# Kernel tuning notes

Measured on AMD Instinct MI355X. Metric: run time of the kernel, lower is better.

The kernel has to match this reference:

```python
import jax, jax.numpy as jnp
import numpy as np

ALPHA, BETA, GAMMA, DELTA = 1.0, 1.0, 1.0, 0.001
DV, DD = 0.5, 1.5
N_INST = 8
EDGES_MAX = 512
EPS = 1e-12


def _safe_norm(sq):
    # sqrt of a sum-of-squares with a tiny eps for grad stability at 0
    return jnp.sqrt(jnp.maximum(sq, 0.0) + EPS)


def _per_image(feat, labels, label_edges):
    # feat: [P, C]; labels, label_edges: [P] int32 in [0, N_INST)
    P, C = feat.shape
    N = N_INST
    counts = jax.ops.segment_sum(jnp.ones((P,), feat.dtype), labels, num_segments=N)  # [N]
    means = jax.ops.segment_sum(feat, labels, num_segments=N) / counts[:, None]       # [N, C]

    # --- variance (pull) loss: per-pixel distance to its cluster mean ---
    d = _safe_norm(jnp.sum((feat - means[labels]) ** 2, axis=-1))  # [P]
    hinge = jax.nn.relu(d - DV) ** 2
    var_loss = jnp.sum(jax.ops.segment_sum(hinge, labels, num_segments=N) / counts) / N

    # --- distance (push) loss between cluster means, upper triangle ---
    diff = means[:, None, :] - means[None, :, :]
    dm = _safe_norm(jnp.sum(diff ** 2, axis=-1))  # [N, N]
    triu = jnp.triu(jnp.ones((N, N), dtype=bool), k=1)
    dist_loss = jnp.sum(jnp.where(triu, jax.nn.relu(2.0 * DD - dm) ** 2, 0.0)) / (N * (N - 1))

    # --- edge loss: first EDGES_MAX boundary pixels per instance (deterministic subsample) ---
    pix = jnp.arange(P, dtype=feat.dtype)
    def first_members(i):
        score = jnp.where(label_edges == i, -pix, -jnp.inf)
        _, idx = jax.lax.top_k(score, EDGES_MAX)
        return idx
    sel = jax.vmap(first_members)(jnp.arange(N))  # [N, E]
    eb = feat[sel.reshape(-1)]                    # [N*E, C]
    sq = jnp.sum(eb ** 2, axis=-1)
    d2 = sq[:, None] + sq[None, :] - 2.0 * (eb @ eb.T)  # [N*E, N*E] squared dists
    pd = _safe_norm(d2)
    pv = jax.nn.relu(2.0 * (DD - DV) - pd) ** 2
    pair = pv.reshape(N, EDGES_MAX, N, EDGES_MAX).sum(axis=(1, 3)) / (EDGES_MAX * EDGES_MAX)
    edge_loss = jnp.sum(jnp.where(triu, pair, 0.0)) / (N * (N - 1))

    # --- regularization on cluster means ---
    reg_loss = jnp.mean(_safe_norm(jnp.sum(means ** 2, axis=-1)))
    return var_loss, dist_loss, edge_loss, reg_loss


def setup_inputs() -> dict:
    key = jax.random.key(0)
    k1, k2, k3 = jax.random.split(key, 3)
    B, C, H, W = 4, 32, 512, 512
    features = jax.random.normal(k1, (B, C, H, W), jnp.float32)
    labels = jax.random.randint(k2, (B, H, W), 0, N_INST, jnp.int32)
    labelEdges = jax.random.randint(k3, (B, H, W), 0, N_INST, jnp.int32)
    return {"features": features, "labels": labels, "labelEdges": labelEdges}


def reference(features, labels, labelEdges):
    B, C, H, W = features.shape
    feat = features.transpose(0, 2, 3, 1).reshape(B, H * W, C)
    lab = labels.reshape(B, -1)
    le = labelEdges.reshape(B, -1)
    v, d, e, r = jax.vmap(_per_image)(feat, lab, le)
    varLoss = ALPHA * jnp.sum(v)
    distLoss = BETA * jnp.sum(d)
    edgeLoss = GAMMA * jnp.sum(e)
    regLoss = DELTA * jnp.sum(r)
    totalLoss = varLoss + distLoss + edgeLoss + regLoss
    return (totalLoss, varLoss, distLoss, edgeLoss, regLoss)
```

## Files before the change

### kernel.cpp

```cpp
#include <hip/hip_runtime.h>

#define NB 4
#define NC 32
#define NPIX 262144
#define NI 8
#define NE 512
#define FEPS 1e-12f

#define WS_SUMS   0
#define WS_CNT    1024
#define WS_HINGE  1056
#define WS_EDGE   1088
#define WS_ZERO_N 1089
#define WS_SEL    2048
#define WS_EB     20480
#define WS_SQ     544768

typedef __bf16 bf16x8 __attribute__((ext_vector_type(8)));
typedef float  f32x4  __attribute__((ext_vector_type(4)));

static __device__ __forceinline__ unsigned short f2bf(float x) {
    unsigned u = __builtin_bit_cast(unsigned, x);
    u += 0x7FFF + ((u >> 16) & 1);
    return (unsigned short)(u >> 16);
}

__global__ __launch_bounds__(256) void k_zero(float* __restrict__ ws) {
    int i = blockIdx.x * 256 + threadIdx.x;
    if (i < WS_ZERO_N) ws[i] = 0.f;
}

__global__ __launch_bounds__(256, 2) void k_seg_sums(const float* __restrict__ feat,
                                                     const int* __restrict__ lab,
                                                     float* __restrict__ sums,
                                                     float* __restrict__ cnts) {
    int tid = threadIdx.x;
    int lane = tid & 63, w = tid >> 6;
    int b = blockIdx.x >> 8, cb = blockIdx.x & 255;
    const float* fb = feat + ((size_t)b * NC + w * 8) * NPIX + cb * 1024;
    const int*   lb = lab + (size_t)b * NPIX + cb * 1024;

    float r[64];
#pragma unroll
    for (int k = 0; k < 64; k++) r[k] = 0.f;
    float cnt[8] = {0.f, 0.f, 0.f, 0.f, 0.f, 0.f, 0.f, 0.f};

#pragma unroll 1
    for (int g = 0; g < 4; g++) {
        int idx = g * 256 + lane * 4;
        int4 lv = *(const int4*)(lb + idx);
        float4 msk[8];
#pragma unroll
        for (int bin = 0; bin < 8; bin++) {
            msk[bin].x = (lv.x == bin) ? 1.f : 0.f;
            msk[bin].y = (lv.y == bin) ? 1.f : 0.f;
            msk[bin].z = (lv.z == bin) ? 1.f : 0.f;
            msk[bin].w = (lv.w == bin) ? 1.f : 0.f;
        }
        if (w == 0) {
#pragma unroll
            for (int bin = 0; bin < 8; bin++)
                cnt[bin] += msk[bin].x + msk[bin].y + msk[bin].z + msk[bin].w;
        }
#pragma unroll
        for (int c = 0; c < 8; c++) {
            float4 f = *(const float4*)(fb + (size_t)c * NPIX + idx);
#pragma unroll
            for (int bin = 0; bin < 8; bin++)
                r[c * 8 + bin] += msk[bin].x * f.x + msk[bin].y * f.y
                                + msk[bin].z * f.z + msk[bin].w * f.w;
        }
    }

#pragma unroll
    for (int half = 32; half >= 1; half >>= 1) {
#pragma unroll
        for (int k = 0; k < half; k++) {
            float t0 = __shfl_xor(r[k], half);
            float t1 = __shfl_xor(r[k + half], half);
            r[k] = (lane & half) ? (r[k + half] + t1) : (r[k] + t0);
        }
    }
    atomicAdd(&sums[((size_t)b * NI + (lane & 7)) * NC + w * 8 + (lane >> 3)], r[0]);

    if (w == 0) {
#pragma unroll
        for (int m = 8; m <= 32; m <<= 1) {
#pragma unroll
            for (int bin = 0; bin < 8; bin++) cnt[bin] += __shfl_xor(cnt[bin], m);
        }
#pragma unroll
        for (int half = 4; half >= 1; half >>= 1) {
#pragma unroll
            for (int k = 0; k < half; k++) {
                float t0 = __shfl_xor(cnt[k], half);
                float t1 = __shfl_xor(cnt[k + half], half);
                cnt[k] = (lane & half) ? (cnt[k + half] + t1) : (cnt[k] + t0);
            }
        }
        if (lane < 8) atomicAdd(&cnts[b * NI + lane], cnt[0]);
    }
}

__global__ __launch_bounds__(256, 4) void k_var(const float* __restrict__ feat,
                                                const int* __restrict__ lab,
                                                const float* __restrict__ sums,
                                                const float* __restrict__ cnts,
                                                float* __restrict__ hinge) {
    __shared__ float mlds[NI][33];
    __shared__ float hred[4][8];
    int tid = threadIdx.x;
    int lane = tid & 63, w = tid >> 6;
    int b = blockIdx.x >> 8, cb = blockIdx.x & 255;
    {
        int i = tid >> 5, c = tid & 31;
        mlds[i][c] = sums[(b * NI + i) * NC + c] / cnts[b * NI + i];
    }
    __syncthreads();

    int idx = tid * 4;
    int4 lv = *(const int4*)(lab + (size_t)b * NPIX + cb * 1024 + idx);
    const float* fb = feat + (size_t)b * NC * NPIX + cb * 1024 + idx;
    float ax = 0.f, ay = 0.f, az = 0.f, aw = 0.f;
#pragma unroll 1
    for (int cc = 0; cc < NC; cc += 8) {
        float4 f[8];
#pragma unroll
        for (int u = 0; u < 8; u++) f[u] = *(const float4*)(fb + (size_t)(cc + u) * NPIX);
#pragma unroll
        for (int u = 0; u < 8; u++) {
            int c = cc + u;
            float d;
            d = f[u].x - mlds[lv.x][c]; ax += d * d;
            d = f[u].y - mlds[lv.y][c]; ay += d * d;
            d = f[u].z - mlds[lv.z][c]; az += d * d;
            d = f[u].w - mlds[lv.w][c]; aw += d * d;
        }
    }
    float t;
    t = fmaxf(sqrtf(ax + FEPS) - 0.5f, 0.f); float hx = t * t;
    t = fmaxf(sqrtf(ay + FEPS) - 0.5f, 0.f); float hy = t * t;
    t = fmaxf(sqrtf(az + FEPS) - 0.5f, 0.f); float hz = t * t;
    t = fmaxf(sqrtf(aw + FEPS) - 0.5f, 0.f); float hw = t * t;

    float hacc[8];
#pragma unroll
    for (int bin = 0; bin < 8; bin++)
        hacc[bin] = ((lv.x == bin) ? hx : 0.f) + ((lv.y == bin) ? hy : 0.f)
                  + ((lv.z == bin) ? hz : 0.f) + ((lv.w == bin) ? hw : 0.f);
#pragma unroll
    for (int m = 8; m <= 32; m <<= 1) {
#pragma unroll
        for (int bin = 0; bin < 8; bin++) hacc[bin] += __shfl_xor(hacc[bin], m);
    }
#pragma unroll
    for (int half = 4; half >= 1; half >>= 1) {
#pragma unroll
        for (int k = 0; k < half; k++) {
            float t0 = __shfl_xor(hacc[k], half);
            float t1 = __shfl_xor(hacc[k + half], half);
            hacc[k] = (lane & half) ? (hacc[k + half] + t1) : (hacc[k] + t0);
        }
    }
    if (lane < 8) hred[w][lane] = hacc[0];
    __syncthreads();
    if (tid < 8)
        atomicAdd(&hinge[b * NI + tid],
                  hred[0][tid] + hred[1][tid] + hred[2][tid] + hred[3][tid]);
}

__global__ __launch_bounds__(64) void k_sel(const int* __restrict__ le, int* __restrict__ sel) {
    int inst = blockIdx.x & 7;
    int b = blockIdx.x >> 3;
    int lane = threadIdx.x;
    const int* lp = le + (size_t)b * NPIX;
    int* sp = sel + blockIdx.x * NE;
    int s = 0;
    for (int base = 0; base < NPIX && s < NE; base += 256) {
        int4 l = *(const int4*)(lp + base + lane * 4);
        int m0 = (l.x == inst), m1 = (l.y == inst), m2 = (l.z == inst), m3 = (l.w == inst);
        int cnt = m0 + m1 + m2 + m3;
        int incl = cnt;
#pragma unroll
        for (int off = 1; off < 64; off <<= 1) {
            int t = __shfl_up(incl, off);
            if (lane >= off) incl += t;
        }
        int r = incl - cnt;
        int pbase = base + lane * 4;
        if (m0) { if (s + r < NE) sp[s + r] = pbase + 0; r++; }
        if (m1) { if (s + r < NE) sp[s + r] = pbase + 1; r++; }
        if (m2) { if (s + r < NE) sp[s + r] = pbase + 2; r++; }
        if (m3) { if (s + r < NE) sp[s + r] = pbase + 3; r++; }
        s += __shfl(incl, 63);
    }
    for (int idx = s + lane; idx < NE; idx += 64) sp[idx] = 0;
}

__global__ __launch_bounds__(256) void k_gather(const float* __restrict__ feat,
                                                const int* __restrict__ sel,
                                                short* __restrict__ ebh,
                                                float* __restrict__ sq) {
    int bi = blockIdx.x;
    int b = bi >> 3;
    int tid = threadIdx.x;
#pragma unroll
    for (int half = 0; half < 2; half++) {
        int r = bi * NE + half * 256 + tid;
        int p = sel[r];
        const float* fp = feat + (size_t)b * NC * NPIX + p;
        float s = 0.f;
        int pk[16];
#pragma unroll
        for (int c2 = 0; c2 < 16; c2++) {
            float v0 = fp[(size_t)(2 * c2) * NPIX];
            float v1 = fp[(size_t)(2 * c2 + 1) * NPIX];
            s += v0 * v0 + v1 * v1;
            pk[c2] = (unsigned)f2bf(v0) | ((unsigned)f2bf(v1) << 16);
        }
        sq[r] = s;
        int4* dst = (int4*)(ebh + (size_t)r * NC);
        dst[0] = make_int4(pk[0], pk[1], pk[2], pk[3]);
        dst[1] = make_int4(pk[4], pk[5], pk[6], pk[7]);
        dst[2] = make_int4(pk[8], pk[9], pk[10], pk[11]);
        dst[3] = make_int4(pk[12], pk[13], pk[14], pk[15]);
    }
}

__global__ __launch_bounds__(256) void k_edge(const short* __restrict__ ebh,
                                              const float* __restrict__ sq,
                                              float* __restrict__ edge_acc) {
    __shared__ float sqa[128], sqb[128];
    __shared__ float wsum[4];
    int tid = threadIdx.x;
    int lane = tid & 63, w = tid >> 6;
    int ti = blockIdx.x >> 2, tj = blockIdx.x & 3;
    int q = blockIdx.y;
    int b = blockIdx.z;
    int pi = 0, pj = 0, k = q;
    for (int i = 0; i < 8; i++) { int row = 7 - i; if (k < row) { pi = i; pj = i + 1 + k; break; } k -= row; }
    int base_a = b * 4096 + pi * NE + ti * 128;
    int base_b = b * 4096 + pj * NE + tj * 128;

    if (tid < 128) sqa[tid] = sq[base_a + tid];
    else sqb[tid - 128] = sq[base_b + tid - 128];
    __syncthreads();

    int lrow = lane & 15;
    int lk = (lane >> 4) * 8;

    bf16x8 a[2];
#pragma unroll
    for (int u = 0; u < 2; u++)
        a[u] = *(const bf16x8*)(ebh + (size_t)(base_a + w * 32 + u * 16 + lrow) * NC + lk);
    bf16x8 bb[8];
#pragma unroll
    for (int v = 0; v < 8; v++)
        bb[v] = *(const bf16x8*)(ebh + (size_t)(base_b + v * 16 + lrow) * NC + lk);

    f32x4 acc[2][8];
#pragma unroll
    for (int u = 0; u < 2; u++)
#pragma unroll
        for (int v = 0; v < 8; v++) acc[u][v] = (f32x4){0.f, 0.f, 0.f, 0.f};

#pragma unroll
    for (int u = 0; u < 2; u++)
#pragma unroll
        for (int v = 0; v < 8; v++)
            acc[u][v] = __builtin_amdgcn_mfma_f32_16x16x32_bf16(a[u], bb[v], acc[u][v], 0, 0, 0);

    float lsum = 0.f;
    int orow0 = w * 32 + (lane >> 4) * 4;
    int ocol = lane & 15;
#pragma unroll
    for (int u = 0; u < 2; u++) {
#pragma unroll
        for (int v = 0; v < 8; v++) {
            float sb = sqb[v * 16 + ocol];
#pragma unroll
            for (int rg = 0; rg < 4; rg++) {
                float d2 = sqa[orow0 + u * 16 + rg] + sb - 2.f * acc[u][v][rg];
                float pd = sqrtf(fmaxf(d2, 0.f) + FEPS);
                float t = 2.f - pd;
                if (t > 0.f) lsum += t * t;
            }
        }
    }
#pragma unroll
    for (int off = 32; off > 0; off >>= 1) lsum += __shfl_xor(lsum, off);
    if (lane == 0) wsum[w] = lsum;
    __syncthreads();
    if (tid == 0) atomicAdd(edge_acc, wsum[0] + wsum[1] + wsum[2] + wsum[3]);
}

__global__ __launch_bounds__(256) void k_final(const float* __restrict__ sums,
                                               const float* __restrict__ cnts,
                                               const float* __restrict__ hinge,
                                               const float* __restrict__ edge_acc,
                                               float* __restrict__ out) {
    __shared__ float m[NB * NI * NC];
    __shared__ float accs[3];
    int tid = threadIdx.x;
    if (tid < 3) accs[tid] = 0.f;
    for (int i = tid; i < NB * NI * NC; i += 256) m[i] = sums[i] / cnts[i >> 5];
    __syncthreads();

    float var_p = 0.f, dist_p = 0.f, reg_p = 0.f;
    if (tid < 32) {
        var_p = hinge[tid] / cnts[tid] * (1.f / 8.f);
        const float* mm = &m[tid * NC];
        float s = 0.f;
        for (int c = 0; c < NC; c++) s += mm[c] * mm[c];
        reg_p = sqrtf(s + FEPS) * (0.001f / 8.f);
    }
    if (tid < NB * 28) {
        int b = tid / 28, q = tid % 28;
        int pi = 0, pj = 0, k = q;
        for (int i = 0; i < 8; i++) { int row = 7 - i; if (k < row) { pi = i; pj = i + 1 + k; break; } k -= row; }
        const float* ma = &m[(b * NI + pi) * NC];
        const float* mb = &m[(b * NI + pj) * NC];
        float s = 0.f;
        for (int c = 0; c < NC; c++) { float d = ma[c] - mb[c]; s += d * d; }
        float dm = sqrtf(s + FEPS);
        float t = fmaxf(3.0f - dm, 0.f);
        dist_p = t * t * (1.f / 56.f);
    }
    atomicAdd(&accs[0], var_p);
    atomicAdd(&accs[1], dist_p);
    atomicAdd(&accs[2], reg_p);
    __syncthreads();
    if (tid == 0) {
        float var = accs[0], dist = accs[1], reg = accs[2];
        float edge = edge_acc[0] * (1.f / (512.f * 512.f * 56.f));
        out[0] = var + dist + edge + reg;
        out[1] = var;
        out[2] = dist;
        out[3] = edge;
        out[4] = reg;
    }
}

extern "C" void kernel_launch(void* const* d_in, const int* in_sizes, int n_in,
                              void* d_out, int out_size, void* d_ws, size_t ws_size,
                              hipStream_t stream) {
    const float* feat   = (const float*)d_in[0];
    const int*   labels = (const int*)d_in[1];
    const int*   le     = (const int*)d_in[2];
    float* out = (float*)d_out;
    float* ws  = (float*)d_ws;

    float* sums  = ws + WS_SUMS;
    float* cnts  = ws + WS_CNT;
    float* hinge = ws + WS_HINGE;
    float* edge  = ws + WS_EDGE;
    int*   sel   = (int*)(ws + WS_SEL);
    short* ebh   = (short*)(ws + WS_EB);
    float* sq    = ws + WS_SQ;

    hipLaunchKernelGGL(k_zero,     dim3(5),           dim3(256), 0, stream, ws);
    hipLaunchKernelGGL(k_seg_sums, dim3(1024),        dim3(256), 0, stream, feat, labels, sums, cnts);
    hipLaunchKernelGGL(k_var,      dim3(1024),        dim3(256), 0, stream, feat, labels, sums, cnts, hinge);
    hipLaunchKernelGGL(k_sel,      dim3(32),          dim3(64),  0, stream, le, sel);
    hipLaunchKernelGGL(k_gather,   dim3(32),          dim3(256), 0, stream, feat, sel, ebh, sq);
    hipLaunchKernelGGL(k_edge,     dim3(16, 28, 4),   dim3(256), 0, stream, ebh, sq, edge);
    hipLaunchKernelGGL(k_final,    dim3(1),           dim3(256), 0, stream, sums, cnts, hinge, edge, out);
}
```

Baseline: 309.9 us.

## Split segment-sum channels across more blocks, prefetch feature loads, widen gather grid

k_seg_sums now splits the 32 channels into two halves across twice as many blocks, using 32 accumulators per thread instead of 64. It allows 4 waves per SIMD via launch bounds and software-prefetches the next pixel group's labels and features. k_var double-buffers its channel loads so the next 8 channels are in flight while the current ones are consumed. k_gather spreads each row's 32 channels over 4 threads with a shuffle reduction, and launches 8x more blocks to hide gather latency. The cost is extra label reads and more atomics in seg_sums, plus higher register pressure from the prefetch buffers.

New measurement: 318.3 us. 2.7% more time.

```diff
diff --git a/kernel.cpp b/kernel.cpp
--- a/kernel.cpp
+++ b/kernel.cpp
@@ -30,50 +30,67 @@
     if (i < WS_ZERO_N) ws[i] = 0.f;
 }
 
-__global__ __launch_bounds__(256, 2) void k_seg_sums(const float* __restrict__ feat,
+__global__ __launch_bounds__(256, 4) void k_seg_sums(const float* __restrict__ feat,
                                                      const int* __restrict__ lab,
                                                      float* __restrict__ sums,
                                                      float* __restrict__ cnts) {
     int tid = threadIdx.x;
     int lane = tid & 63, w = tid >> 6;
-    int b = blockIdx.x >> 8, cb = blockIdx.x & 255;
-    const float* fb = feat + ((size_t)b * NC + w * 8) * NPIX + cb * 1024;
+    int blk = blockIdx.x;
+    int b = blk >> 9, rem = blk & 511;
+    int cb = rem >> 1, h = rem & 1;
+    int ch0 = h * 16 + w * 4;
+    const float* fb = feat + ((size_t)b * NC + ch0) * NPIX + cb * 1024;
     const int*   lb = lab + (size_t)b * NPIX + cb * 1024;
-
-    float r[64];
-#pragma unroll
-    for (int k = 0; k < 64; k++) r[k] = 0.f;
+    bool docnt = (w == 0) && (h == 0);
+
+    float r[32];
+#pragma unroll
+    for (int k = 0; k < 32; k++) r[k] = 0.f;
     float cnt[8] = {0.f, 0.f, 0.f, 0.f, 0.f, 0.f, 0.f, 0.f};
 
-#pragma unroll 1
+#define ACC_ELEM(lx, v0, v1, v2, v3)                         \
+    do {                                                     \
+        _Pragma("unroll")                                    \
+        for (int bin = 0; bin < 8; ++bin) {                  \
+            float mk = ((lx) == bin) ? 1.f : 0.f;            \
+            if (docnt) cnt[bin] += mk;                       \
+            r[bin]      += mk * (v0);                        \
+            r[8 + bin]  += mk * (v1);                        \
+            r[16 + bin] += mk * (v2);                        \
+            r[24 + bin] += mk * (v3);                        \
+        }                                                    \
+    } while (0)
+
+    int4   lvA = *(const int4*)(lb + lane * 4);
+    float4 fA0 = *(const float4*)(fb + 0 * (size_t)NPIX + lane * 4);
+    float4 fA1 = *(const float4*)(fb + 1 * (size_t)NPIX + lane * 4);
+    float4 fA2 = *(const float4*)(fb + 2 * (size_t)NPIX + lane * 4);
+    float4 fA3 = *(const float4*)(fb + 3 * (size_t)NPIX + lane * 4);
+
+#pragma unroll
     for (int g = 0; g < 4; g++) {
-        int idx = g * 256 + lane * 4;
-        int4 lv = *(const int4*)(lb + idx);
-        float4 msk[8];
-#pragma unroll
-        for (int bin = 0; bin < 8; bin++) {
-            msk[bin].x = (lv.x == bin) ? 1.f : 0.f;
-            msk[bin].y = (lv.y == bin) ? 1.f : 0.f;
-            msk[bin].z = (lv.z == bin) ? 1.f : 0.f;
-            msk[bin].w = (lv.w == bin) ? 1.f : 0.f;
-        }
-        if (w == 0) {
-#pragma unroll
-            for (int bin = 0; bin < 8; bin++)
-                cnt[bin] += msk[bin].x + msk[bin].y + msk[bin].z + msk[bin].w;
-        }
-#pragma unroll
-        for (int c = 0; c < 8; c++) {
-            float4 f = *(const float4*)(fb + (size_t)c * NPIX + idx);
-#pragma unroll
-            for (int bin = 0; bin < 8; bin++)
-                r[c * 8 + bin] += msk[bin].x * f.x + msk[bin].y * f.y
-                                + msk[bin].z * f.z + msk[bin].w * f.w;
-        }
-    }
-
-#pragma unroll
-    for (int half = 32; half >= 1; half >>= 1) {
+        int4 lvC = lvA;
+        float4 c0 = fA0, c1 = fA1, c2 = fA2, c3 = fA3;
+        if (g < 3) {
+            int idx = (g + 1) * 256 + lane * 4;
+            lvA = *(const int4*)(lb + idx);
+            fA0 = *(const float4*)(fb + 0 * (size_t)NPIX + idx);
+            fA1 = *(const float4*)(fb + 1 * (size_t)NPIX + idx);
+            fA2 = *(const float4*)(fb + 2 * (size_t)NPIX + idx);
+            fA3 = *(const float4*)(fb + 3 * (size_t)NPIX + idx);
+        }
+        ACC_ELEM(lvC.x, c0.x, c1.x, c2.x, c3.x);
+        ACC_ELEM(lvC.y, c0.y, c1.y, c2.y, c3.y);
+        ACC_ELEM(lvC.z, c0.z, c1.z, c2.z, c3.z);
+        ACC_ELEM(lvC.w, c0.w, c1.w, c2.w, c3.w);
+    }
+#undef ACC_ELEM
+
+#pragma unroll
+    for (int k = 0; k < 32; k++) r[k] += __shfl_xor(r[k], 32);
+#pragma unroll
+    for (int half = 16; half >= 1; half >>= 1) {
 #pragma unroll
         for (int k = 0; k < half; k++) {
             float t0 = __shfl_xor(r[k], half);
@@ -81,9 +98,10 @@
             r[k] = (lane & half) ? (r[k + half] + t1) : (r[k] + t0);
         }
     }
-    atomicAdd(&sums[((size_t)b * NI + (lane & 7)) * NC + w * 8 + (lane >> 3)], r[0]);
-
-    if (w == 0) {
+    if (lane < 32)
+        atomicAdd(&sums[((size_t)b * NI + (lane & 7)) * NC + ch0 + (lane >> 3)], r[0]);
+
+    if (docnt) {
 #pragma unroll
         for (int m = 8; m <= 32; m <<= 1) {
 #pragma unroll
@@ -122,21 +140,35 @@
     int4 lv = *(const int4*)(lab + (size_t)b * NPIX + cb * 1024 + idx);
     const float* fb = feat + (size_t)b * NC * NPIX + cb * 1024 + idx;
     float ax = 0.f, ay = 0.f, az = 0.f, aw = 0.f;
-#pragma unroll 1
-    for (int cc = 0; cc < NC; cc += 8) {
-        float4 f[8];
-#pragma unroll
-        for (int u = 0; u < 8; u++) f[u] = *(const float4*)(fb + (size_t)(cc + u) * NPIX);
-#pragma unroll
-        for (int u = 0; u < 8; u++) {
-            int c = cc + u;
-            float d;
-            d = f[u].x - mlds[lv.x][c]; ax += d * d;
-            d = f[u].y - mlds[lv.y][c]; ay += d * d;
-            d = f[u].z - mlds[lv.z][c]; az += d * d;
-            d = f[u].w - mlds[lv.w][c]; aw += d * d;
-        }
-    }
+
+    float4 FA[8], FB[8];
+#define LOADF(BUF, CC)                                                          \
+    do {                                                                        \
+        _Pragma("unroll")                                                       \
+        for (int u = 0; u < 8; ++u)                                             \
+            BUF[u] = *(const float4*)(fb + (size_t)((CC) + u) * NPIX);          \
+    } while (0)
+#define CONSUME(BUF, CC)                                                        \
+    do {                                                                        \
+        _Pragma("unroll")                                                       \
+        for (int u = 0; u < 8; ++u) {                                           \
+            int c = (CC) + u;                                                   \
+            float d;                                                            \
+            d = BUF[u].x - mlds[lv.x][c]; ax += d * d;                          \
+            d = BUF[u].y - mlds[lv.y][c]; ay += d * d;                          \
+            d = BUF[u].z - mlds[lv.z][c]; az += d * d;                          \
+            d = BUF[u].w - mlds[lv.w][c]; aw += d * d;                          \
+        }                                                                       \
+    } while (0)
+
+    LOADF(FA, 0);
+    LOADF(FB, 8);  CONSUME(FA, 0);
+    LOADF(FA, 16); CONSUME(FB, 8);
+    LOADF(FB, 24); CONSUME(FA, 16);
+    CONSUME(FB, 24);
+#undef LOADF
+#undef CONSUME
+
     float t;
     t = fmaxf(sqrtf(ax + FEPS) - 0.5f, 0.f); float hx = t * t;
     t = fmaxf(sqrtf(ay + FEPS) - 0.5f, 0.f); float hy = t * t;
@@ -201,30 +233,28 @@
                                                 const int* __restrict__ sel,
                                                 short* __restrict__ ebh,
                                                 float* __restrict__ sq) {
-    int bi = blockIdx.x;
+    int oct = blockIdx.x;
+    int bi = blockIdx.y;
     int b = bi >> 3;
     int tid = threadIdx.x;
-#pragma unroll
-    for (int half = 0; half < 2; half++) {
-        int r = bi * NE + half * 256 + tid;
-        int p = sel[r];
-        const float* fp = feat + (size_t)b * NC * NPIX + p;
-        float s = 0.f;
-        int pk[16];
-#pragma unroll
-        for (int c2 = 0; c2 < 16; c2++) {
-            float v0 = fp[(size_t)(2 * c2) * NPIX];
-            float v1 = fp[(size_t)(2 * c2 + 1) * NPIX];
-            s += v0 * v0 + v1 * v1;
-            pk[c2] = (unsigned)f2bf(v0) | ((unsigned)f2bf(v1) << 16);
-        }
-        sq[r] = s;
-        int4* dst = (int4*)(ebh + (size_t)r * NC);
-        dst[0] = make_int4(pk[0], pk[1], pk[2], pk[3]);
-        dst[1] = make_int4(pk[4], pk[5], pk[6], pk[7]);
-        dst[2] = make_int4(pk[8], pk[9], pk[10], pk[11]);
-        dst[3] = make_int4(pk[12], pk[13], pk[14], pk[15]);
-    }
+    int rrel = tid >> 2, qc = tid & 3;
+    int r = bi * NE + oct * 64 + rrel;
+    int p = sel[r];
+    const float* fp = feat + (size_t)b * NC * NPIX + p;
+    int c0 = qc * 8;
+    float s = 0.f;
+    int pk[4];
+#pragma unroll
+    for (int j = 0; j < 4; j++) {
+        float v0 = fp[(size_t)(c0 + 2 * j) * NPIX];
+        float v1 = fp[(size_t)(c0 + 2 * j + 1) * NPIX];
+        s += v0 * v0 + v1 * v1;
+        pk[j] = (unsigned)f2bf(v0) | ((unsigned)f2bf(v1) << 16);
+    }
+    *(int4*)(ebh + (size_t)r * NC + c0) = make_int4(pk[0], pk[1], pk[2], pk[3]);
+    s += __shfl_xor(s, 1);
+    s += __shfl_xor(s, 2);
+    if (qc == 0) sq[r] = s;
 }
 
 __global__ __launch_bounds__(256) void k_edge(const short* __restrict__ ebh,
@@ -359,10 +389,10 @@
     float* sq    = ws + WS_SQ;
 
     hipLaunchKernelGGL(k_zero,     dim3(5),           dim3(256), 0, stream, ws);
-    hipLaunchKernelGGL(k_seg_sums, dim3(1024),        dim3(256), 0, stream, feat, labels, sums, cnts);
+    hipLaunchKernelGGL(k_seg_sums, dim3(2048),        dim3(256), 0, stream, feat, labels, sums, cnts);
     hipLaunchKernelGGL(k_var,      dim3(1024),        dim3(256), 0, stream, feat, labels, sums, cnts, hinge);
     hipLaunchKernelGGL(k_sel,      dim3(32),          dim3(64),  0, stream, le, sel);
-    hipLaunchKernelGGL(k_gather,   dim3(32),          dim3(256), 0, stream, feat, sel, ebh, sq);
+    hipLaunchKernelGGL(k_gather,   dim3(8, 32),       dim3(256), 0, stream, feat, sel, ebh, sq);
     hipLaunchKernelGGL(k_edge,     dim3(16, 28, 4),   dim3(256), 0, stream, ebh, sq, edge);
     hipLaunchKernelGGL(k_final,    dim3(1),           dim3(256), 0, stream, sums, cnts, hinge, edge, out);
 }
```
